# Kernel tuning notes

Hardware: AMD Instinct MI355X
Metric: run time of the kernel (lower is better)

Reference implementation:

```python
import jax, jax.numpy as jnp
import numpy as np

C = 768
H = 12
HD = C // H
SCALE = HD ** -0.5
EPS = 1e-5


def setup_inputs() -> dict:
    key = jax.random.key(0)
    kit = iter(jax.random.split(key, 40))
    r = lambda *s: jax.random.normal(next(kit), s, jnp.float32) * 0.02
    d = dict(
        s_x=jax.random.normal(next(kit), (8, 196, C), jnp.float32),
        t_x=jax.random.normal(next(kit), (8, 1568, C), jnp.float32),
        ln1s_g=jnp.ones(C), ln1s_b=jnp.zeros(C),
        mha_w=r(3 * C, C), mha_b=r(3 * C), mha_ow=r(C, C), mha_ob=r(C),
        ln1t_g=jnp.ones(C), ln1t_b=jnp.zeros(C),
        attn_qkv_w=r(3 * C, C), attn_q_b=r(C), attn_v_b=r(C), attn_pw=r(C, C), attn_pb=r(C),
        lnt2s_g=jnp.ones(C), lnt2s_b=jnp.zeros(C),
        t2s_qw=r(C, C), t2s_qb=r(C), t2s_kvw=r(2 * C, C), t2s_kvb=r(C), t2s_pw=r(C, C), t2s_pb=r(C),
        lns2t_g=jnp.ones(C), lns2t_b=jnp.zeros(C),
        s2t_qw=r(C, C), s2t_qb=r(C), s2t_kvw=r(2 * C, C), s2t_kvb=r(C), s2t_pw=r(C, C), s2t_pb=r(C),
        ln2s_g=jnp.ones(C), ln2s_b=jnp.zeros(C),
        cfc_w=r(4 * C, C), cfc_b=r(4 * C), cproj_w=r(C, 4 * C), cproj_b=r(C),
        ln2t_g=jnp.ones(C), ln2t_b=jnp.zeros(C),
        fc1_w=r(4 * C, C), fc1_b=r(4 * C), fc2_w=r(C, 4 * C), fc2_b=r(C),
    )
    return d


def ln(x, g, b):
    m = x.mean(-1, keepdims=True)
    v = jnp.mean((x - m) ** 2, -1, keepdims=True)
    return (x - m) * jax.lax.rsqrt(v + EPS) * g + b


def heads(x):  # (B, N, C) -> (B, H, N, HD)
    B, N, _ = x.shape
    return x.reshape(B, N, H, HD).transpose(0, 2, 1, 3)


def mhsa(q, k, v):  # (B, H, Nq, HD), (B, H, Nk, HD) -> (B, Nq, C)
    a = jax.nn.softmax(jnp.einsum('bhqd,bhkd->bhqk', q * SCALE, k), axis=-1)
    o = jnp.einsum('bhqk,bhkd->bhqd', a, v)
    B, _, Nq, _ = o.shape
    return o.transpose(0, 2, 1, 3).reshape(B, Nq, C)


def reference(s_x, t_x, ln1s_g, ln1s_b, mha_w, mha_b, mha_ow, mha_ob,
              ln1t_g, ln1t_b, attn_qkv_w, attn_q_b, attn_v_b, attn_pw, attn_pb,
              lnt2s_g, lnt2s_b, t2s_qw, t2s_qb, t2s_kvw, t2s_kvb, t2s_pw, t2s_pb,
              lns2t_g, lns2t_b, s2t_qw, s2t_qb, s2t_kvw, s2t_kvb, s2t_pw, s2t_pb,
              ln2s_g, ln2s_b, cfc_w, cfc_b, cproj_w, cproj_b,
              ln2t_g, ln2t_b, fc1_w, fc1_b, fc2_w, fc2_b):
    # 1) clip self-attention. torch nn.MultiheadAttention (batch_first=False)
    # treats axis 0 of the (B, s_N, C) input as the sequence dim, so we
    # faithfully attend over the batch axis.
    y = ln(s_x, ln1s_g, ln1s_b)
    qkv = y @ mha_w.T + mha_b  # (B, s_N, 3C)
    q, k, v = jnp.split(qkv, 3, axis=-1)
    qt, kt, vt = (a.transpose(1, 0, 2) for a in (q, k, v))  # (s_N, B, C)
    o = mhsa(heads(qt), heads(kt), heads(vt))  # (s_N, B, C)
    o = o @ mha_ow.T + mha_ob
    s_x = s_x + o.transpose(1, 0, 2)

    # 2) video-stream self-attention (qkv_bias=True -> cat(q_b, 0, v_b))
    y = ln(t_x, ln1t_g, ln1t_b)
    qkv_bias = jnp.concatenate([attn_q_b, jnp.zeros_like(attn_v_b), attn_v_b])
    qkv = y @ attn_qkv_w.T + qkv_bias
    q, k, v = jnp.split(qkv, 3, axis=-1)
    o = mhsa(heads(q), heads(k), heads(v))
    t_x = t_x + (o @ attn_pw.T + attn_pb)

    # 3) T2S cross: query from LN(s_x), key/value from (updated, un-normed) t_x
    ys = ln(s_x, lnt2s_g, lnt2s_b)
    q = ys @ t2s_qw.T + t2s_qb
    kv = t_x @ t2s_kvw.T + jnp.concatenate([jnp.zeros_like(t2s_kvb), t2s_kvb])
    k, v = jnp.split(kv, 2, axis=-1)
    o = mhsa(heads(q), heads(k), heads(v))
    s_x = s_x + (o @ t2s_pw.T + t2s_pb)

    # 4) S2T cross: query from LN(t_x), key/value from updated s_x
    yt = ln(t_x, lns2t_g, lns2t_b)
    q = yt @ s2t_qw.T + s2t_qb
    kv = s_x @ s2t_kvw.T + jnp.concatenate([jnp.zeros_like(s2t_kvb), s2t_kvb])
    k, v = jnp.split(kv, 2, axis=-1)
    o = mhsa(heads(q), heads(k), heads(v))
    t_x = t_x + (o @ s2t_pw.T + s2t_pb)

    # 5) clip MLP (QuickGELU)
    y = ln(s_x, ln2s_g, ln2s_b)
    h = y @ cfc_w.T + cfc_b
    h = h * jax.nn.sigmoid(1.702 * h)
    s_x = s_x + (h @ cproj_w.T + cproj_b)

    # 6) video MLP (exact GELU, torch default)
    y = ln(t_x, ln2t_g, ln2t_b)
    h = jax.nn.gelu(y @ fc1_w.T + fc1_b, approximate=False)
    t_x = t_x + (h @ fc2_w.T + fc2_b)
    return (s_x, t_x)
```

## Files before the change

kernel.cpp:

```cpp
#include <hip/hip_runtime.h>
#include <stdint.h>


typedef uint16_t u16;
typedef uint16_t u16x8 __attribute__((ext_vector_type(8)));
typedef uint16_t u16x4 __attribute__((ext_vector_type(4)));
typedef short bf16x8 __attribute__((ext_vector_type(8)));
typedef float f32x4 __attribute__((ext_vector_type(4)));

__device__ __forceinline__ float b2f(u16 u) {
    union { float f; uint32_t i; } x;
    x.i = ((uint32_t)u) << 16;
    return x.f;
}
__device__ __forceinline__ u16 f2b(float f) {
    union { float f; uint32_t i; } x;
    x.f = f;
    uint32_t i = x.i;
    uint32_t r = (i + 0x7FFFu + ((i >> 16) & 1u)) >> 16;
    return (u16)r;
}
__device__ __forceinline__ u16 f2b_trunc(float f) {
    union { float f; uint32_t i; } x;
    x.f = f;
    return (u16)(x.i >> 16);
}

__device__ __forceinline__ void gload16(const u16* g, u16* l) {
    __builtin_amdgcn_global_load_lds(
        (const __attribute__((address_space(1))) uint32_t*)g,
        (__attribute__((address_space(3))) uint32_t*)l, 16, 0, 0);
}

struct CvtAll {
    const float* s[14];
    u16* d[14];
    int cum[15];
};
__global__ __launch_bounds__(256) void cvt_all(CvtAll c) {
    int i = blockIdx.x * 256 + threadIdx.x;
    if (i >= c.cum[14]) return;
    int seg = 0;
    #pragma unroll
    for (int k = 1; k < 14; k++) seg += (i >= c.cum[k]);
    int j = i - c.cum[seg];
    c.d[seg][j] = f2b(c.s[seg][j]);
}

__global__ __launch_bounds__(256) void build_bias_pool(float* __restrict__ dst,
    const float* mha_b, const float* attn_q_b, const float* attn_v_b,
    const float* mha_ob, const float* attn_pb, const float* t2s_kvb,
    const float* t2s_qb, const float* t2s_pb, const float* s2t_qb,
    const float* s2t_kvb, const float* s2t_pb, const float* cfc_b,
    const float* cproj_b, const float* fc1_b, const float* fc2_b) {
    int i = blockIdx.x * 256 + threadIdx.x;
    float v = 0.f;
    if (i < 2304) v = mha_b[i];
    else if (i < 4608) { int j = i - 2304; v = (j < 768) ? attn_q_b[j] : (j < 1536 ? 0.f : attn_v_b[j - 1536]); }
    else if (i < 5376) v = mha_ob[i - 4608];
    else if (i < 6144) v = attn_pb[i - 5376];
    else if (i < 7680) { int j = i - 6144; v = (j < 768) ? 0.f : t2s_kvb[j - 768]; }
    else if (i < 8448) v = t2s_qb[i - 7680];
    else if (i < 9216) v = t2s_pb[i - 8448];
    else if (i < 9984) v = s2t_qb[i - 9216];
    else if (i < 11520) { int j = i - 9984; v = (j < 768) ? 0.f : s2t_kvb[j - 768]; }
    else if (i < 12288) v = s2t_pb[i - 11520];
    else if (i < 15360) v = cfc_b[i - 12288];
    else if (i < 16128) v = cproj_b[i - 15360];
    else if (i < 19200) v = fc1_b[i - 16128];
    else if (i < 19968) v = fc2_b[i - 19200];
    else return;
    dst[i] = v;
}

__device__ __forceinline__ float block_sum(float v, float* red) {
    #pragma unroll
    for (int o = 32; o > 0; o >>= 1) v += __shfl_down(v, o, 64);
    int w = threadIdx.x >> 6, l = threadIdx.x & 63;
    __syncthreads();
    if (l == 0) red[w] = v;
    __syncthreads();
    return red[0] + red[1] + red[2] + red[3];
}

__device__ __forceinline__ void ln_row(const float* xr, const float* g,
                                       const float* bta, u16* yr, float* red) {
    const int t = threadIdx.x;
    float v0 = xr[t], v1 = xr[t + 256], v2 = xr[t + 512];
    float mean = block_sum(v0 + v1 + v2, red) * (1.0f / 768.0f);
    float d0 = v0 - mean, d1 = v1 - mean, d2 = v2 - mean;
    float var = block_sum(d0 * d0 + d1 * d1 + d2 * d2, red) * (1.0f / 768.0f);
    float rs = rsqrtf(var + 1e-5f);
    yr[t]       = f2b(d0 * rs * g[t]       + bta[t]);
    yr[t + 256] = f2b(d1 * rs * g[t + 256] + bta[t + 256]);
    yr[t + 512] = f2b(d2 * rs * g[t + 512] + bta[t + 512]);
}

__global__ __launch_bounds__(256) void ln_dual(
    const float* __restrict__ x, int rows0,
    const float* g0, const float* b0, u16* y0,
    const float* g1, const float* b1, u16* y1) {
    __shared__ float red[4];
    int r = blockIdx.x;
    if (r < rows0) ln_row(x + (size_t)r * 768, g0, b0, y0 + (size_t)r * 768, red);
    else ln_row(x + (size_t)r * 768, g1, b1, y1 + (size_t)(r - rows0) * 768, red);
}

__global__ __launch_bounds__(256) void ln_dual_in(
    const float* __restrict__ xs, const float* __restrict__ xt,
    float* __restrict__ xcopy, int rows0,
    const float* g0, const float* b0, u16* y0,
    const float* g1, const float* b1, u16* y1) {
    __shared__ float red[4];
    int r = blockIdx.x, t = threadIdx.x;
    const float* xr; const float* g; const float* bta; u16* yr;
    if (r < rows0) { xr = xs + (size_t)r * 768; g = g0; bta = b0; yr = y0 + (size_t)r * 768; }
    else { xr = xt + (size_t)(r - rows0) * 768; g = g1; bta = b1; yr = y1 + (size_t)(r - rows0) * 768; }
    float v0 = xr[t], v1 = xr[t + 256], v2 = xr[t + 512];
    float* xc = xcopy + (size_t)r * 768;
    xc[t] = v0; xc[t + 256] = v1; xc[t + 512] = v2;
    float mean = block_sum(v0 + v1 + v2, red) * (1.0f / 768.0f);
    float d0 = v0 - mean, d1 = v1 - mean, d2 = v2 - mean;
    float var = block_sum(d0 * d0 + d1 * d1 + d2 * d2, red) * (1.0f / 768.0f);
    float rs = rsqrtf(var + 1e-5f);
    yr[t]       = f2b(d0 * rs * g[t]       + bta[t]);
    yr[t + 256] = f2b(d1 * rs * g[t + 256] + bta[t + 256]);
    yr[t + 512] = f2b(d2 * rs * g[t + 512] + bta[t + 512]);
}

struct TransP {
    const u16* vp; u16* vt;
    int Nk, Nkp, gx, nb;
    long long vA, vJ;
};
__device__ __forceinline__ void transpose_body(const TransP p, int bid, u16 (*T)[72]) {
    const int x = bid % p.gx, inst = bid / p.gx;
    const int a = inst / 12, h = inst % 12;
    const int t0 = x * 64;
    const int tid = threadIdx.x;
    const int kvl = tid >> 2, dseg = (tid & 3) * 16;
    u16x8 v0 = {}, v1 = {};
    if (t0 + kvl < p.Nk) {
        const u16* src = p.vp + a * p.vA + (long long)(t0 + kvl) * p.vJ + h * 64 + dseg;
        v0 = *(const u16x8*)src;
        v1 = *(const u16x8*)(src + 8);
    }
    *(u16x8*)&T[kvl][dseg]     = v0;
    *(u16x8*)&T[kvl][dseg + 8] = v1;
    __syncthreads();
    const int dl = tid >> 2, kseg = (tid & 3) * 16;
    u16x8 w0, w1;
    #pragma unroll
    for (int j = 0; j < 8; j++) w0[j] = T[kseg + j][dl];
    #pragma unroll
    for (int j = 0; j < 8; j++) w1[j] = T[kseg + 8 + j][dl];
    u16* orow = p.vt + ((size_t)inst * 64 + dl) * p.Nkp + t0 + kseg;
    *(u16x8*)orow = w0;
    *(u16x8*)(orow + 8) = w1;
}
__global__ __launch_bounds__(256) void transpose_pair(TransP p0, TransP p1) {
    __shared__ u16 T[64][72];
    int bid = blockIdx.x;
    if (bid < p0.nb) transpose_body(p0, bid, T);
    else transpose_body(p1, bid - p0.nb, T);
}

struct GemmP {
    const u16* A; const u16* W; const float* bias;
    u16* Cb; float* Cf;
    int M, N, K, gx, nb;
};
template <int MODE, int BM>
__device__ __forceinline__ void gemm_body(const GemmP p, int bid,
                                          u16 (*AsF)[32], u16 (*BsF)[32]) {
    constexpr int MI = BM / 32;
    const int tid = threadIdx.x;
    const int lane = tid & 63;
    const int wid = tid >> 6;
    const int wr = (wid >> 1) * (BM / 2), wc = (wid & 1) * 64;
    const int bx = bid % p.gx, by = bid / p.gx;
    const int m0 = bx * BM, n0 = by * 128;
    const int lr = lane >> 2, lc = (lane & 3) * 8;
    const int fr = lane & 15, fk = (lane >> 4) * 8;
    const int abase = wid * (BM / 4);
    const int bbase = wid * 32;
    f32x4 acc[MI][4] = {};
    for (int k0 = 0; k0 < p.K; k0 += 64) {
        #pragma unroll
        for (int s = 0; s < 2; s++) {
            #pragma unroll
            for (int j = 0; j < BM / 64; j++) {
                int rowa = m0 + abase + j * 16 + lr;
                rowa = rowa < p.M ? rowa : p.M - 1;
                gload16(p.A + (size_t)rowa * p.K + k0 + s * 32 + lc,
                        &AsF[s * 128 + abase + j * 16][0]);
            }
            #pragma unroll
            for (int j = 0; j < 2; j++) {
                gload16(p.W + (size_t)(n0 + bbase + j * 16 + lr) * p.K + k0 + s * 32 + lc,
                        &BsF[s * 128 + bbase + j * 16][0]);
            }
        }
        __syncthreads();
        #pragma unroll
        for (int s = 0; s < 2; s++) {
            bf16x8 a[MI], b[4];
            #pragma unroll
            for (int i = 0; i < MI; i++) a[i] = *(const bf16x8*)&AsF[s * 128 + wr + i * 16 + fr][fk];
            #pragma unroll
            for (int j = 0; j < 4; j++) b[j] = *(const bf16x8*)&BsF[s * 128 + wc + j * 16 + fr][fk];
            #pragma unroll
            for (int i = 0; i < MI; i++)
                #pragma unroll
                for (int j = 0; j < 4; j++)
                    acc[i][j] = __builtin_amdgcn_mfma_f32_16x16x32_bf16(a[i], b[j], acc[i][j], 0, 0, 0);
        }
        __syncthreads();
    }
    const int er = (lane >> 4) * 4;
    #pragma unroll
    for (int i = 0; i < MI; i++) {
        #pragma unroll
        for (int reg = 0; reg < 4; reg++) {
            int r = m0 + wr + i * 16 + er + reg;
            if (r >= p.M) continue;
            #pragma unroll
            for (int j = 0; j < 4; j++) {
                int c = n0 + wc + j * 16 + fr;
                float v = acc[i][j][reg] + p.bias[c];
                size_t idx = (size_t)r * p.N + c;
                if (MODE == 1) {
                    p.Cf[idx] += v;
                } else if (MODE == 4) {
                    float nv = p.Cf[idx] + v;
                    p.Cf[idx] = nv;
                    p.Cb[idx] = f2b(nv);
                } else {
                    if (MODE == 2) v = v / (1.0f + expf(-1.702f * v));
                    if (MODE == 3) v = 0.5f * v * (1.0f + erff(v * 0.70710678118654752f));
                    p.Cb[idx] = f2b(v);
                }
            }
        }
    }
}
template <int M0, int B0, int M1, int B1>
__global__ __launch_bounds__(256) void gemm_pair(GemmP p0, GemmP p1) {
    __shared__ u16 As[2 * 128][32];
    __shared__ u16 Bs[2 * 128][32];
    int bid = blockIdx.x;
    if (bid < p0.nb) gemm_body<M0, B0>(p0, bid, As, Bs);
    else gemm_body<M1, B1>(p1, bid - p0.nb, As, Bs);
}
template <int M0, int B0, int M1, int B1>
__global__ __launch_bounds__(256) void gemm2_trans(GemmP p0, GemmP p1, TransP t0) {
    __shared__ u16 As[2 * 128][32];
    __shared__ u16 Bs[2 * 128][32];
    int bid = blockIdx.x;
    if (bid < p0.nb) gemm_body<M0, B0>(p0, bid, As, Bs);
    else if (bid < p0.nb + p1.nb) gemm_body<M1, B1>(p1, bid - p0.nb, As, Bs);
    else transpose_body(t0, bid - p0.nb - p1.nb, (u16(*)[72])&As[0][0]);
}

template <int MODE>
__global__ __launch_bounds__(512) void gemm256(
    const u16* __restrict__ A, const u16* __restrict__ W,
    const float* __restrict__ bias, u16* __restrict__ Cb,
    float* __restrict__ Cf, int M, int N, int K) {
    __shared__ u16 LA[2][256][64];
    __shared__ u16 LB[2][256][64];
    const int tid = threadIdx.x;
    const int lane = tid & 63, wid = tid >> 6;
    const int wm = wid >> 2, wn = wid & 3;
    int nwg = gridDim.x;
    int q = nwg >> 3, r8 = nwg & 7;
    int xcd = blockIdx.x & 7, orig = blockIdx.x >> 3;
    int bid = (xcd < r8 ? xcd * (q + 1) : r8 * (q + 1) + (xcd - r8) * q) + orig;
    const int gx = M >> 8;
    const int bx = bid % gx, by = bid / gx;
    const int m0 = bx * 256, n0 = by * 256;
    const int srow = tid >> 3;
    const int sgcol = ((tid & 7) * 8) ^ (((tid >> 3) & 7) << 3);
    const u16* Ag = A + (size_t)m0 * K;
    const u16* Bg = W + (size_t)n0 * K;
    const int fr = lane & 15, g = lane >> 4, fk = g * 8;
    const int rsw = (fr & 7) << 3;

    auto stageHalf = [&](u16* half, const u16* gsrc, int rowOff, int kc) {
        #pragma unroll
        for (int c = 0; c < 2; c++) {
            int row = rowOff + c * 64 + srow;
            gload16(gsrc + (size_t)row * K + kc + sgcol,
                    half + c * 4096 + wid * 512);
        }
    };
    auto stage1 = [&](int s, int kc, int which) {
        if (which == 0) stageHalf(&LB[s][0][0],   Bg, 0,   kc);
        else if (which == 1) stageHalf(&LB[s][128][0], Bg, 128, kc);
        else if (which == 2) stageHalf(&LA[s][0][0],   Ag, 0,   kc);
        else stageHalf(&LA[s][128][0], Ag, 128, kc);
    };

    f32x4 acc[8][4] = {};
    const int NT = K >> 6;
    stage1(0, 0, 0); stage1(0, 0, 1); stage1(0, 0, 2); stage1(0, 0, 3);

    for (int kt = 0; kt < NT; kt++) {
        const int cur = kt & 1;
        const int kn = (kt + 1) << 6;
        const bool pf = (kt + 1 < NT);
        asm volatile("s_waitcnt vmcnt(2)" ::: "memory");
        __builtin_amdgcn_s_barrier();
        bf16x8 bfr[4][2];
        #pragma unroll
        for (int fj = 0; fj < 4; fj++)
            #pragma unroll
            for (int ks = 0; ks < 2; ks++)
                bfr[fj][ks] = *(const bf16x8*)&LB[cur][wn * 64 + fj * 16 + fr][(ks * 32 + fk) ^ rsw];
        #pragma unroll
        for (int ph = 0; ph < 2; ph++) {
            bf16x8 afr[2][2];
            #pragma unroll
            for (int i2 = 0; i2 < 2; i2++)
                #pragma unroll
                for (int ks = 0; ks < 2; ks++)
                    afr[i2][ks] = *(const bf16x8*)&LA[cur][(ph * 2 + i2) * 32 + wm * 16 + fr][(ks * 32 + fk) ^ rsw];
            if (pf) stage1(cur ^ 1, kn, ph);
            __builtin_amdgcn_s_setprio(1);
            #pragma unroll
            for (int i2 = 0; i2 < 2; i2++)
                #pragma unroll
                for (int ks = 0; ks < 2; ks++)
                    #pragma unroll
                    for (int fj = 0; fj < 4; fj++)
                        acc[ph * 2 + i2][fj] = __builtin_amdgcn_mfma_f32_16x16x32_bf16(
                            afr[i2][ks], bfr[fj][ks], acc[ph * 2 + i2][fj], 0, 0, 0);
            __builtin_amdgcn_s_setprio(0);
        }
        if (pf) asm volatile("s_waitcnt vmcnt(4)" ::: "memory");
        else    asm volatile("s_waitcnt vmcnt(0)" ::: "memory");
        __builtin_amdgcn_s_barrier();
        #pragma unroll
        for (int ph = 2; ph < 4; ph++) {
            bf16x8 afr[2][2];
            #pragma unroll
            for (int i2 = 0; i2 < 2; i2++)
                #pragma unroll
                for (int ks = 0; ks < 2; ks++)
                    afr[i2][ks] = *(const bf16x8*)&LA[cur][(ph * 2 + i2) * 32 + wm * 16 + fr][(ks * 32 + fk) ^ rsw];
            if (pf) stage1(cur ^ 1, kn, ph);
            __builtin_amdgcn_s_setprio(1);
            #pragma unroll
            for (int i2 = 0; i2 < 2; i2++)
                #pragma unroll
                for (int ks = 0; ks < 2; ks++)
                    #pragma unroll
                    for (int fj = 0; fj < 4; fj++)
                        acc[ph * 2 + i2][fj] = __builtin_amdgcn_mfma_f32_16x16x32_bf16(
                            afr[i2][ks], bfr[fj][ks], acc[ph * 2 + i2][fj], 0, 0, 0);
            __builtin_amdgcn_s_setprio(0);
        }
    }
    const int er = g * 4;
    #pragma unroll
    for (int fi = 0; fi < 8; fi++) {
        #pragma unroll
        for (int reg = 0; reg < 4; reg++) {
            int rr = m0 + fi * 32 + wm * 16 + er + reg;
            #pragma unroll
            for (int fj = 0; fj < 4; fj++) {
                int c = n0 + wn * 64 + fj * 16 + fr;
                float v = acc[fi][fj][reg] + bias[c];
                size_t idx = (size_t)rr * N + c;
                if (MODE == 1) {
                    Cf[idx] += v;
                } else if (MODE == 4) {
                    float nv = Cf[idx] + v;
                    Cf[idx] = nv;
                    Cb[idx] = f2b(nv);
                } else {
                    if (MODE == 2) v = v / (1.0f + expf(-1.702f * v));
                    if (MODE == 3) v = 0.5f * v * (1.0f + erff(v * 0.70710678118654752f));
                    Cb[idx] = f2b(v);
                }
            }
        }
    }
}

struct FlashP {
    const u16* qp; const u16* kp; const u16* vt; u16* op;
    int Nq, Nk, Nkp, gx, nb;
    long long qA, qI, kA, kJ, oA, oI;
};
__device__ __forceinline__ void flash_body(const FlashP p, int bid,
    u16 (*Ks)[64][64], u16 (*Vs)[64][64], u16 (*Ps)[16][64]) {
    const int x = bid % p.gx, inst = bid / p.gx;
    const int a = inst / 12, h = inst % 12;
    const int tid = threadIdx.x, lane = tid & 63, w = tid >> 6;
    const int fr = lane & 15, g = lane >> 4, fk = g * 8;
    const int f3s = (fr & 7) << 3;
    const u16* qb = p.qp + a * p.qA + h * 64;
    const u16* kb = p.kp + a * p.kA + h * 64;
    const u16* vtb = p.vt + (size_t)inst * 64 * p.Nkp;
    const int q0 = x * 64 + w * 16;

    bf16x8 qf[2];
    {
        u16x8 raw0 = {}, raw1 = {};
        int qr = q0 + fr;
        if (qr < p.Nq) {
            const u16* qrp = qb + (long long)qr * p.qI;
            raw0 = *(const u16x8*)(qrp + fk);
            raw1 = *(const u16x8*)(qrp + 32 + fk);
        }
        const float QS = 0.125f * 1.44269504088896340736f;
        u16x8 s0, s1;
        #pragma unroll
        for (int e = 0; e < 8; e++) {
            s0[e] = f2b(b2f(raw0[e]) * QS);
            s1[e] = f2b(b2f(raw1[e]) * QS);
        }
        qf[0] = *(bf16x8*)&s0;
        qf[1] = *(bf16x8*)&s1;
    }
    float mrun = -1e30f, lrun = 0.f;
    f32x4 o[4] = {};

    const int l = lane;
    const int srow = w * 8 + (l >> 3);
    const int sdcol = ((l & 7) * 8) ^ (((l >> 3) & 7) << 3);

    auto STAGE = [&](int s, int t0) {
        #pragma unroll
        for (int c = 0; c < 2; c++) {
            int row = c * 32 + srow;
            int kr = t0 + row; if (kr >= p.Nk) kr = p.Nk - 1;
            gload16(kb + (long long)kr * p.kJ + sdcol, &Ks[s][0][0] + c * 2048 + w * 512);
            gload16(vtb + (size_t)row * p.Nkp + t0 + sdcol, &Vs[s][0][0] + c * 2048 + w * 512);
        }
    };

    const int nt = (p.Nk + 63) >> 6;
    STAGE(0, 0);
    for (int it = 0; it < nt; ++it) {
        const int t0 = it << 6;
        const int cur = it & 1;
        if (it + 1 < nt) {
            STAGE(cur ^ 1, t0 + 64);
            asm volatile("s_waitcnt vmcnt(4)" ::: "memory");
        } else {
            asm volatile("s_waitcnt vmcnt(0)" ::: "memory");
        }
        __builtin_amdgcn_s_barrier();

        f32x4 s[4] = {};
        __builtin_amdgcn_s_setprio(1);
        #pragma unroll
        for (int hh = 0; hh < 4; hh++) {
            bf16x8 k0f = *(const bf16x8*)&Ks[cur][hh * 16 + fr][fk ^ f3s];
            bf16x8 k1f = *(const bf16x8*)&Ks[cur][hh * 16 + fr][(32 + fk) ^ f3s];
            s[hh] = __builtin_amdgcn_mfma_f32_16x16x32_bf16(k0f, qf[0], s[hh], 0, 0, 0);
            s[hh] = __builtin_amdgcn_mfma_f32_16x16x32_bf16(k1f, qf[1], s[hh], 0, 0, 0);
        }
        __builtin_amdgcn_s_setprio(0);

        if (t0 + 64 > p.Nk) {
            #pragma unroll
            for (int hh = 0; hh < 4; hh++)
                #pragma unroll
                for (int r = 0; r < 4; r++)
                    if (t0 + hh * 16 + 4 * g + r >= p.Nk) s[hh][r] = -1e30f;
        }
        float a0 = fmaxf(fmaxf(s[0][0], s[0][1]), s[0][2]);
        float a1 = fmaxf(fmaxf(s[0][3], s[1][0]), s[1][1]);
        float a2 = fmaxf(fmaxf(s[1][2], s[1][3]), s[2][0]);
        float a3 = fmaxf(fmaxf(s[2][1], s[2][2]), s[2][3]);
        float a4 = fmaxf(fmaxf(s[3][0], s[3][1]), s[3][2]);
        float b0 = fmaxf(fmaxf(a0, a1), a2);
        float b1 = fmaxf(fmaxf(a3, a4), s[3][3]);
        float lmax = fmaxf(b0, b1);
        lmax = fmaxf(lmax, __shfl_xor(lmax, 16, 64));
        lmax = fmaxf(lmax, __shfl_xor(lmax, 32, 64));
        if (!__all(lmax <= mrun + 8.0f)) {
            float mn = fmaxf(mrun, lmax);
            float sf = exp2f(mrun - mn);
            mrun = mn;
            lrun *= sf;
            float sfo[4];
            #pragma unroll
            for (int r = 0; r < 4; r++) sfo[r] = __shfl(sf, g * 4 + r, 64);
            #pragma unroll
            for (int dt = 0; dt < 4; dt++)
                #pragma unroll
                for (int r = 0; r < 4; r++) o[dt][r] *= sfo[r];
        }
        float pp[4][4];
        float ps = 0.f;
        #pragma unroll
        for (int hh = 0; hh < 4; hh++)
            #pragma unroll
            for (int r = 0; r < 4; r++) {
                pp[hh][r] = exp2f(s[hh][r] - mrun);
                ps += pp[hh][r];
            }
        ps += __shfl_xor(ps, 16, 64);
        ps += __shfl_xor(ps, 32, 64);
        lrun += ps;
        #pragma unroll
        for (int hh = 0; hh < 4; hh++) {
            u16x4 pk;
            #pragma unroll
            for (int r = 0; r < 4; r++) pk[r] = f2b_trunc(pp[hh][r]);
            *(u16x4*)&Ps[w][fr][(hh * 16 + g * 4) ^ f3s] = pk;
        }
        bf16x8 pa0 = *(const bf16x8*)&Ps[w][fr][fk ^ f3s];
        bf16x8 pa1 = *(const bf16x8*)&Ps[w][fr][(32 + fk) ^ f3s];
        __builtin_amdgcn_s_setprio(1);
        #pragma unroll
        for (int dt = 0; dt < 4; dt++) {
            bf16x8 vf0 = *(const bf16x8*)&Vs[cur][dt * 16 + fr][fk ^ f3s];
            bf16x8 vf1 = *(const bf16x8*)&Vs[cur][dt * 16 + fr][(32 + fk) ^ f3s];
            o[dt] = __builtin_amdgcn_mfma_f32_16x16x32_bf16(pa0, vf0, o[dt], 0, 0, 0);
            o[dt] = __builtin_amdgcn_mfma_f32_16x16x32_bf16(pa1, vf1, o[dt], 0, 0, 0);
        }
        __builtin_amdgcn_s_setprio(0);
        __builtin_amdgcn_s_barrier();
    }
    float rcp = 1.0f / lrun;
    #pragma unroll
    for (int r = 0; r < 4; r++) {
        float rr = __shfl(rcp, g * 4 + r, 64);
        int qq = q0 + g * 4 + r;
        if (qq >= p.Nq) continue;
        u16* orow = p.op + a * p.oA + (long long)qq * p.oI + h * 64;
        #pragma unroll
        for (int dt = 0; dt < 4; dt++)
            orow[dt * 16 + fr] = f2b(o[dt][r] * rr);
    }
}
__global__ __launch_bounds__(256) void flash_pair(FlashP p0, FlashP p1) {
    __shared__ u16 Ks[2][64][64];
    __shared__ u16 Vs[2][64][64];
    __shared__ u16 Ps[4][16][64];
    int bid = blockIdx.x;
    if (bid < p0.nb) flash_body(p0, bid, Ks, Vs, Ps);
    else flash_body(p1, bid - p0.nb, Ks, Vs, Ps);
}

extern "C" void kernel_launch(void* const* d_in, const int* in_sizes, int n_in,
                              void* d_out, int out_size, void* d_ws, size_t ws_size,
                              hipStream_t stream) {
    const int B = 8, sN = 196, tN = 1568;
    const int Ms = B * sN;
    const int Mt = B * tN;
    const int n_sf = Ms * 768;
    const int n_tf = Mt * 768;
    (void)n_in; (void)out_size; (void)ws_size;

    const bool dict_order = (in_sizes[0] == n_sf);
    auto IN = [&](int di, int ai) -> const float* {
        return (const float*)d_in[dict_order ? di : ai];
    };
    const float* in_sx      = IN(0, 35);
    const float* in_tx      = IN(1, 42);
    const float* ln1s_g     = IN(2, 14);
    const float* ln1s_b     = IN(3, 13);
    const float* mha_w      = IN(4, 28);
    const float* mha_b      = IN(5, 25);
    const float* mha_ow     = IN(6, 27);
    const float* mha_ob     = IN(7, 26);
    const float* ln1t_g     = IN(8, 16);
    const float* ln1t_b     = IN(9, 15);
    const float* attn_qkv_w = IN(10, 3);
    const float* attn_q_b   = IN(11, 2);
    const float* attn_v_b   = IN(12, 4);
    const float* attn_pw    = IN(13, 1);
    const float* attn_pb    = IN(14, 0);
    const float* lnt2s_g    = IN(15, 24);
    const float* lnt2s_b    = IN(16, 23);
    const float* t2s_qw     = IN(17, 41);
    const float* t2s_qb     = IN(18, 40);
    const float* t2s_kvw    = IN(19, 37);
    const float* t2s_kvb    = IN(20, 36);
    const float* t2s_pw     = IN(21, 39);
    const float* t2s_pb     = IN(22, 38);
    const float* lns2t_g    = IN(23, 22);
    const float* lns2t_b    = IN(24, 21);
    const float* s2t_qw     = IN(25, 34);
    const float* s2t_qb     = IN(26, 33);
    const float* s2t_kvw    = IN(27, 30);
    const float* s2t_kvb    = IN(28, 29);
    const float* s2t_pw     = IN(29, 32);
    const float* s2t_pb     = IN(30, 31);
    const float* ln2s_g     = IN(31, 18);
    const float* ln2s_b     = IN(32, 17);
    const float* cfc_w      = IN(33, 6);
    const float* cfc_b      = IN(34, 5);
    const float* cproj_w    = IN(35, 8);
    const float* cproj_b    = IN(36, 7);
    const float* ln2t_g     = IN(37, 20);
    const float* ln2t_b     = IN(38, 19);
    const float* fc1_w      = IN(39, 10);
    const float* fc1_b      = IN(40, 9);
    const float* fc2_w      = IN(41, 12);
    const float* fc2_b      = IN(42, 11);

    float* s_f = (float*)d_out;
    float* t_f = (float*)d_out + n_sf;

    char* ws = (char*)d_ws;
    size_t off = 0;
    auto take = [&](size_t bytes) { size_t o = off; off += (bytes + 255) & ~(size_t)255; return o; };
    float* biasP = (float*)(ws + take(19968 * 4));
    u16*   yb    = (u16*)(ws + take((size_t)(Ms + Mt) * 768 * 2));
    u16*   bufA  = (u16*)(ws + take((size_t)Mt * 3072 * 2));
    u16*   bufS  = (u16*)(ws + take((size_t)Mt * 768 * 2));
    u16*   bufB  = (u16*)(ws + take((size_t)Mt * 768 * 2));
    u16*   sxb   = (u16*)(ws + take((size_t)Ms * 768 * 2));
    u16*   vtb_t = (u16*)(ws + take((size_t)96 * 64 * 1600 * 2));
    u16*   yb_s  = yb;
    u16*   yb_t  = yb + (size_t)Ms * 768;
    u16*   vtb_s = yb;
    auto wtake = [&](size_t nelem) { return (u16*)(ws + take(nelem * 2)); };
    u16 *W_mha   = wtake(2304 * 768), *W_mhao  = wtake(768 * 768);
    u16 *W_qkv   = wtake(2304 * 768), *W_attnp = wtake(768 * 768);
    u16 *W_t2sq  = wtake(768 * 768),  *W_t2skv = wtake(1536 * 768), *W_t2sp = wtake(768 * 768);
    u16 *W_s2tq  = wtake(768 * 768),  *W_s2tkv = wtake(1536 * 768), *W_s2tp = wtake(768 * 768);
    u16 *W_cfc   = wtake(3072 * 768), *W_cproj = wtake(768 * 3072);
    u16 *W_fc1   = wtake(3072 * 768), *W_fc2   = wtake(768 * 3072);

    const int B_MHA = 0, B_QKV = 2304, B_MHAO = 4608, B_ATTNP = 5376;
    const int B_T2SKV = 6144, B_T2SQ = 7680, B_T2SP = 8448, B_S2TQ = 9216;
    const int B_S2TKV = 9984, B_S2TP = 11520, B_CFC = 12288, B_CPROJ = 15360;
    const int B_FC1 = 16128, B_FC2 = 19200;

    auto cdiv = [](int a, int b) { return (a + b - 1) / b; };

    {
        CvtAll c;
        const float* ss[14] = { mha_w, mha_ow, attn_qkv_w, attn_pw, t2s_qw, t2s_kvw, t2s_pw,
                                s2t_qw, s2t_kvw, s2t_pw, cfc_w, cproj_w, fc1_w, fc2_w };
        u16* dd[14] = { W_mha, W_mhao, W_qkv, W_attnp, W_t2sq, W_t2skv, W_t2sp,
                        W_s2tq, W_s2tkv, W_s2tp, W_cfc, W_cproj, W_fc1, W_fc2 };
        int nn[14] = { 2304*768, 768*768, 2304*768, 768*768, 768*768, 1536*768, 768*768,
                       768*768, 1536*768, 768*768, 3072*768, 768*3072, 3072*768, 768*3072 };
        int cum = 0;
        for (int k = 0; k < 14; k++) { c.s[k] = ss[k]; c.d[k] = dd[k]; c.cum[k] = cum; cum += nn[k]; }
        c.cum[14] = cum;
        cvt_all<<<cdiv(cum, 256), 256, 0, stream>>>(c);
    }
    build_bias_pool<<<78, 256, 0, stream>>>(biasP,
        mha_b, attn_q_b, attn_v_b, mha_ob, attn_pb, t2s_kvb, t2s_qb, t2s_pb,
        s2t_qb, s2t_kvb, s2t_pb, cfc_b, cproj_b, fc1_b, fc2_b);

    auto GP = [&](const u16* A, const u16* W, const float* bias, u16* Cb, float* Cf,
                  int M, int N, int K, int BM) {
        GemmP p; p.A = A; p.W = W; p.bias = bias; p.Cb = Cb; p.Cf = Cf;
        p.M = M; p.N = N; p.K = K; p.gx = (M + BM - 1) / BM; p.nb = p.gx * (N / 128);
        return p;
    };
    auto FPm = [&](const u16* qp, const u16* kp, const u16* vt, u16* op,
                   int Nq, int Nk, int Nkp, int insts,
                   long long qA, long long qI, long long kA, long long kJ,
                   long long oA, long long oI) {
        FlashP p; p.qp = qp; p.kp = kp; p.vt = vt; p.op = op;
        p.Nq = Nq; p.Nk = Nk; p.Nkp = Nkp; p.gx = (Nq + 63) / 64;
        p.nb = p.gx * insts;
        p.qA = qA; p.qI = qI; p.kA = kA; p.kJ = kJ; p.oA = oA; p.oI = oI;
        return p;
    };
    auto TP = [&](const u16* vp, u16* vt, int Nk, int Nkp, long long vA, long long vJ, int insts) {
        TransP p; p.vp = vp; p.vt = vt; p.Nk = Nk; p.Nkp = Nkp;
        p.gx = (Nk + 63) / 64; p.nb = p.gx * insts; p.vA = vA; p.vJ = vJ;
        return p;
    };

    ln_dual_in<<<Ms + Mt, 256, 0, stream>>>(in_sx, in_tx, (float*)d_out, Ms,
        ln1s_g, ln1s_b, yb_s, ln1t_g, ln1t_b, yb_t);

    gemm256<0><<<49 * (2304 / 256), 512, 0, stream>>>(yb_t, W_qkv, biasP + B_QKV, bufA, (float*)0, Mt, 2304, 768);
    {
        GemmP p0 = GP(yb_s, W_mha, biasP + B_MHA, bufS, 0, Ms, 2304, 768, 64);
        GemmP pz = p0; pz.nb = 0;
        gemm_pair<0, 64, 0, 64><<<p0.nb, 256, 0, stream>>>(p0, pz);
    }
    {
        TransP p0 = TP(bufS + 1536, vtb_s, 8, 64, 2304LL, (long long)sN * 2304, sN * 12);
        TransP p1 = TP(bufA + 1536, vtb_t, tN, 1600, (long long)tN * 2304, 2304LL, B * 12);
        transpose_pair<<<p0.nb + p1.nb, 256, 0, stream>>>(p0, p1);
    }
    {
        FlashP p0 = FPm(bufS, bufS + 768, vtb_s, sxb, 8, 8, 64, sN * 12,
                        2304LL, (long long)sN * 2304, 2304LL, (long long)sN * 2304,
                        768LL, (long long)sN * 768);
        FlashP p1 = FPm(bufA, bufA + 768, vtb_t, bufB, tN, tN, 1600, B * 12,
                        (long long)tN * 2304, 2304LL, (long long)tN * 2304, 2304LL,
                        (long long)tN * 768, 768LL);
        flash_pair<<<p0.nb + p1.nb, 256, 0, stream>>>(p0, p1);
    }
    {
        GemmP p0 = GP(sxb, W_mhao, biasP + B_MHAO, 0, s_f, Ms, 768, 768, 64);
        GemmP p1 = GP(bufB, W_attnp, biasP + B_ATTNP, yb_t, t_f, Mt, 768, 768, 128);
        gemm_pair<1, 64, 4, 128><<<p0.nb + p1.nb, 256, 0, stream>>>(p0, p1);
    }
    ln_dual<<<Ms + Mt, 256, 0, stream>>>((const float*)d_out, Ms,
        lnt2s_g, lnt2s_b, yb_s, lns2t_g, lns2t_b, bufB);
    gemm256<0><<<49 * (1536 / 256), 512, 0, stream>>>(yb_t, W_t2skv, biasP + B_T2SKV, bufA, (float*)0, Mt, 1536, 768);
    {
        GemmP p0 = GP(bufB, W_s2tq, biasP + B_S2TQ, bufS, 0, Mt, 768, 768, 128);
        GemmP p1 = GP(yb_s, W_t2sq, biasP + B_T2SQ, sxb, 0, Ms, 768, 768, 64);
        TransP t0 = TP(bufA + 768, vtb_t, tN, 1600, (long long)tN * 1536, 1536LL, B * 12);
        gemm2_trans<0, 128, 0, 64><<<p0.nb + p1.nb + t0.nb, 256, 0, stream>>>(p0, p1, t0);
    }
    {
        FlashP p0 = FPm(sxb, bufA, vtb_t, yb_s, sN, tN, 1600, B * 12,
                        (long long)sN * 768, 768LL, (long long)tN * 1536, 1536LL,
                        (long long)sN * 768, 768LL);
        FlashP pz = p0; pz.nb = 0;
        flash_pair<<<p0.nb, 256, 0, stream>>>(p0, pz);
    }
    {
        GemmP p0 = GP(yb_s, W_t2sp, biasP + B_T2SP, sxb, s_f, Ms, 768, 768, 64);
        GemmP pz = p0; pz.nb = 0;
        gemm_pair<4, 64, 4, 64><<<p0.nb, 256, 0, stream>>>(p0, pz);
    }
    ln_dual<<<Ms, 256, 0, stream>>>((const float*)d_out, Ms,
        ln2s_g, ln2s_b, yb_s, ln2s_g, ln2s_b, yb_s);
    {
        GemmP p0 = GP(sxb, W_s2tkv, biasP + B_S2TKV, bufB, 0, Ms, 1536, 768, 64);
        GemmP p1 = GP(yb_s, W_cfc, biasP + B_CFC, yb_t, 0, Ms, 3072, 768, 64);
        gemm_pair<0, 64, 2, 64><<<p0.nb + p1.nb, 256, 0, stream>>>(p0, p1);
    }
    {
        GemmP p0 = GP(yb_t, W_cproj, biasP + B_CPROJ, 0, s_f, Ms, 768, 3072, 64);
        GemmP pz = p0; pz.nb = 0;
        TransP t0 = TP(bufB + 768, bufA, sN, 256, (long long)sN * 1536, 1536LL, B * 12);
        gemm2_trans<1, 64, 1, 64><<<p0.nb + t0.nb, 256, 0, stream>>>(p0, pz, t0);
    }
    {
        FlashP p0 = FPm(bufS, bufB, bufA, yb, tN, sN, 256, B * 12,
                        (long long)tN * 768, 768LL, (long long)sN * 1536, 1536LL,
                        (long long)tN * 768, 768LL);
        FlashP pz = p0; pz.nb = 0;
        flash_pair<<<p0.nb, 256, 0, stream>>>(p0, pz);
    }
    {
        GemmP p0 = GP(yb, W_s2tp, biasP + B_S2TP, 0, t_f, Mt, 768, 768, 128);
        GemmP pz = p0; pz.nb = 0;
        gemm_pair<1, 128, 1, 128><<<p0.nb, 256, 0, stream>>>(p0, pz);
    }
    ln_dual<<<Mt, 256, 0, stream>>>(t_f, 0,
        ln2t_g, ln2t_b, yb_t, ln2t_g, ln2t_b, yb_t);
    gemm256<3><<<49 * (3072 / 256), 512, 0, stream>>>(yb_t, W_fc1, biasP + B_FC1, bufA, (float*)0, Mt, 3072, 768);
    {
        GemmP p0 = GP(bufA, W_fc2, biasP + B_FC2, 0, t_f, Mt, 768, 3072, 128);
        GemmP pz = p0; pz.nb = 0;
        gemm_pair<1, 128, 1, 128><<<p0.nb, 256, 0, stream>>>(p0, pz);
    }
}
```

Baseline: 929.6 us.

## Generalize 256x256 GEMM to multi-problem launches with row clamping and use it broadly

Turns the 256x256-tile GEMM into a device body that takes a parameter struct and clamps A rows and masks stores for ragged M. A tri-problem launcher can then batch up to three GEMMs in one grid. Most remaining 128-tile GEMMs (qkv plus mha, the attention projections, t2s kv with the two queries, s2t projection, fc2) move onto it. The V transpose that was fused into a GEMM launch becomes its own launch, and the flash P packing now uses v_cvt_pk_bf16_f32 (round-to-nearest) instead of truncation. Risks include wasted tile work on small M (Ms=1568 rows fits 256 poorly), fewer blocks for N=768 GEMMs, and an extra launch.

```diff
diff --git a/kernel.cpp b/kernel.cpp
--- a/kernel.cpp
+++ b/kernel.cpp
@@ -5,6 +5,7 @@
 typedef uint16_t u16;
 typedef uint16_t u16x8 __attribute__((ext_vector_type(8)));
 typedef uint16_t u16x4 __attribute__((ext_vector_type(4)));
+typedef uint32_t u32x2 __attribute__((ext_vector_type(2)));
 typedef short bf16x8 __attribute__((ext_vector_type(8)));
 typedef float f32x4 __attribute__((ext_vector_type(4)));
 
@@ -19,11 +20,6 @@
     uint32_t i = x.i;
     uint32_t r = (i + 0x7FFFu + ((i >> 16) & 1u)) >> 16;
     return (u16)r;
-}
-__device__ __forceinline__ u16 f2b_trunc(float f) {
-    union { float f; uint32_t i; } x;
-    x.f = f;
-    return (u16)(x.i >> 16);
 }
 
 __device__ __forceinline__ void gload16(const u16* g, u16* l) {
@@ -170,6 +166,7 @@
     u16* Cb; float* Cf;
     int M, N, K, gx, nb;
 };
+
 template <int MODE, int BM>
 __device__ __forceinline__ void gemm_body(const GemmP p, int bid,
                                           u16 (*AsF)[32], u16 (*BsF)[32]) {
@@ -263,42 +260,38 @@
 }
 
 template <int MODE>
-__global__ __launch_bounds__(512) void gemm256(
-    const u16* __restrict__ A, const u16* __restrict__ W,
-    const float* __restrict__ bias, u16* __restrict__ Cb,
-    float* __restrict__ Cf, int M, int N, int K) {
-    __shared__ u16 LA[2][256][64];
-    __shared__ u16 LB[2][256][64];
+__device__ __forceinline__ void g256_body(const GemmP p, int bid, u16* LA, u16* LB) {
     const int tid = threadIdx.x;
     const int lane = tid & 63, wid = tid >> 6;
     const int wm = wid >> 2, wn = wid & 3;
-    int nwg = gridDim.x;
-    int q = nwg >> 3, r8 = nwg & 7;
-    int xcd = blockIdx.x & 7, orig = blockIdx.x >> 3;
-    int bid = (xcd < r8 ? xcd * (q + 1) : r8 * (q + 1) + (xcd - r8) * q) + orig;
-    const int gx = M >> 8;
-    const int bx = bid % gx, by = bid / gx;
+    const int bx = bid % p.gx, by = bid / p.gx;
     const int m0 = bx * 256, n0 = by * 256;
     const int srow = tid >> 3;
     const int sgcol = ((tid & 7) * 8) ^ (((tid >> 3) & 7) << 3);
-    const u16* Ag = A + (size_t)m0 * K;
-    const u16* Bg = W + (size_t)n0 * K;
+    const int K = p.K, M = p.M;
+    const u16* Ag = p.A;
+    const u16* Bg = p.W + (size_t)n0 * K;
     const int fr = lane & 15, g = lane >> 4, fk = g * 8;
     const int rsw = (fr & 7) << 3;
 
-    auto stageHalf = [&](u16* half, const u16* gsrc, int rowOff, int kc) {
-        #pragma unroll
-        for (int c = 0; c < 2; c++) {
-            int row = rowOff + c * 64 + srow;
-            gload16(gsrc + (size_t)row * K + kc + sgcol,
-                    half + c * 4096 + wid * 512);
-        }
-    };
     auto stage1 = [&](int s, int kc, int which) {
-        if (which == 0) stageHalf(&LB[s][0][0],   Bg, 0,   kc);
-        else if (which == 1) stageHalf(&LB[s][128][0], Bg, 128, kc);
-        else if (which == 2) stageHalf(&LA[s][0][0],   Ag, 0,   kc);
-        else stageHalf(&LA[s][128][0], Ag, 128, kc);
+        if (which < 2) {
+            #pragma unroll
+            for (int c = 0; c < 2; c++) {
+                int rl = which * 128 + c * 64 + srow;
+                gload16(Bg + (size_t)rl * K + kc + sgcol,
+                        LB + s * 16384 + which * 8192 + c * 4096 + wid * 512);
+            }
+        } else {
+            int hf = which - 2;
+            #pragma unroll
+            for (int c = 0; c < 2; c++) {
+                int rg = m0 + hf * 128 + c * 64 + srow;
+                rg = rg < M ? rg : M - 1;
+                gload16(Ag + (size_t)rg * K + kc + sgcol,
+                        LA + s * 16384 + hf * 8192 + c * 4096 + wid * 512);
+            }
+        }
     };
 
     f32x4 acc[8][4] = {};
@@ -316,7 +309,7 @@
         for (int fj = 0; fj < 4; fj++)
             #pragma unroll
             for (int ks = 0; ks < 2; ks++)
-                bfr[fj][ks] = *(const bf16x8*)&LB[cur][wn * 64 + fj * 16 + fr][(ks * 32 + fk) ^ rsw];
+                bfr[fj][ks] = *(const bf16x8*)&LB[cur * 16384 + (wn * 64 + fj * 16 + fr) * 64 + ((ks * 32 + fk) ^ rsw)];
         #pragma unroll
         for (int ph = 0; ph < 2; ph++) {
             bf16x8 afr[2][2];
@@ -324,7 +317,7 @@
             for (int i2 = 0; i2 < 2; i2++)
                 #pragma unroll
                 for (int ks = 0; ks < 2; ks++)
-                    afr[i2][ks] = *(const bf16x8*)&LA[cur][(ph * 2 + i2) * 32 + wm * 16 + fr][(ks * 32 + fk) ^ rsw];
+                    afr[i2][ks] = *(const bf16x8*)&LA[cur * 16384 + ((ph * 2 + i2) * 32 + wm * 16 + fr) * 64 + ((ks * 32 + fk) ^ rsw)];
             if (pf) stage1(cur ^ 1, kn, ph);
             __builtin_amdgcn_s_setprio(1);
             #pragma unroll
@@ -347,7 +340,7 @@
             for (int i2 = 0; i2 < 2; i2++)
                 #pragma unroll
                 for (int ks = 0; ks < 2; ks++)
-                    afr[i2][ks] = *(const bf16x8*)&LA[cur][(ph * 2 + i2) * 32 + wm * 16 + fr][(ks * 32 + fk) ^ rsw];
+                    afr[i2][ks] = *(const bf16x8*)&LA[cur * 16384 + ((ph * 2 + i2) * 32 + wm * 16 + fr) * 64 + ((ks * 32 + fk) ^ rsw)];
             if (pf) stage1(cur ^ 1, kn, ph);
             __builtin_amdgcn_s_setprio(1);
             #pragma unroll
@@ -367,25 +360,38 @@
         #pragma unroll
         for (int reg = 0; reg < 4; reg++) {
             int rr = m0 + fi * 32 + wm * 16 + er + reg;
+            if (rr >= M) continue;
             #pragma unroll
             for (int fj = 0; fj < 4; fj++) {
                 int c = n0 + wn * 64 + fj * 16 + fr;
-                float v = acc[fi][fj][reg] + bias[c];
-                size_t idx = (size_t)rr * N + c;
+                float v = acc[fi][fj][reg] + p.bias[c];
+                size_t idx = (size_t)rr * p.N + c;
                 if (MODE == 1) {
-                    Cf[idx] += v;
+                    p.Cf[idx] += v;
                 } else if (MODE == 4) {
-                    float nv = Cf[idx] + v;
-                    Cf[idx] = nv;
-                    Cb[idx] = f2b(nv);
+                    float nv = p.Cf[idx] + v;
+                    p.Cf[idx] = nv;
+                    p.Cb[idx] = f2b(nv);
                 } else {
                     if (MODE == 2) v = v / (1.0f + expf(-1.702f * v));
                     if (MODE == 3) v = 0.5f * v * (1.0f + erff(v * 0.70710678118654752f));
-                    Cb[idx] = f2b(v);
+                    p.Cb[idx] = f2b(v);
                 }
             }
         }
     }
+}
+template <int M0, int M1, int M2>
+__global__ __launch_bounds__(512) void gemm256_tri(GemmP p0, GemmP p1, GemmP p2) {
+    __shared__ u16 LA[2 * 256 * 64];
+    __shared__ u16 LB[2 * 256 * 64];
+    int nwg = gridDim.x;
+    int q = nwg >> 3, r8 = nwg & 7;
+    int xcd = blockIdx.x & 7, orig = blockIdx.x >> 3;
+    int bid = (xcd < r8 ? xcd * (q + 1) : r8 * (q + 1) + (xcd - r8) * q) + orig;
+    if (bid < p0.nb) g256_body<M0>(p0, bid, LA, LB);
+    else if (bid < p0.nb + p1.nb) g256_body<M1>(p1, bid - p0.nb, LA, LB);
+    else g256_body<M2>(p2, bid - p0.nb - p1.nb, LA, LB);
 }
 
 struct FlashP {
@@ -509,10 +515,11 @@
         lrun += ps;
         #pragma unroll
         for (int hh = 0; hh < 4; hh++) {
-            u16x4 pk;
-            #pragma unroll
-            for (int r = 0; r < 4; r++) pk[r] = f2b_trunc(pp[hh][r]);
-            *(u16x4*)&Ps[w][fr][(hh * 16 + g * 4) ^ f3s] = pk;
+            uint32_t plo, phi;
+            asm("v_cvt_pk_bf16_f32 %0, %1, %2" : "=v"(plo) : "v"(pp[hh][0]), "v"(pp[hh][1]));
+            asm("v_cvt_pk_bf16_f32 %0, %1, %2" : "=v"(phi) : "v"(pp[hh][2]), "v"(pp[hh][3]));
+            u32x2 pk; pk[0] = plo; pk[1] = phi;
+            *(u32x2*)&Ps[w][fr][(hh * 16 + g * 4) ^ f3s] = pk;
         }
         bf16x8 pa0 = *(const bf16x8*)&Ps[w][fr][fk ^ f3s];
         bf16x8 pa1 = *(const bf16x8*)&Ps[w][fr][(32 + fk) ^ f3s];
@@ -660,6 +667,13 @@
         p.M = M; p.N = N; p.K = K; p.gx = (M + BM - 1) / BM; p.nb = p.gx * (N / 128);
         return p;
     };
+    auto GP256 = [&](const u16* A, const u16* W, const float* bias, u16* Cb, float* Cf,
+                     int M, int N, int K) {
+        GemmP p; p.A = A; p.W = W; p.bias = bias; p.Cb = Cb; p.Cf = Cf;
+        p.M = M; p.N = N; p.K = K; p.gx = (M + 255) / 256; p.nb = p.gx * (N / 256);
+        return p;
+    };
+    auto ZERO = [&](GemmP p) { GemmP z = p; z.nb = 0; return z; };
     auto FPm = [&](const u16* qp, const u16* kp, const u16* vt, u16* op,
                    int Nq, int Nk, int Nkp, int insts,
                    long long qA, long long qI, long long kA, long long kJ,
@@ -679,11 +693,10 @@
     ln_dual_in<<<Ms + Mt, 256, 0, stream>>>(in_sx, in_tx, (float*)d_out, Ms,
         ln1s_g, ln1s_b, yb_s, ln1t_g, ln1t_b, yb_t);
 
-    gemm256<0><<<49 * (2304 / 256), 512, 0, stream>>>(yb_t, W_qkv, biasP + B_QKV, bufA, (float*)0, Mt, 2304, 768);
-    {
-        GemmP p0 = GP(yb_s, W_mha, biasP + B_MHA, bufS, 0, Ms, 2304, 768, 64);
-        GemmP pz = p0; pz.nb = 0;
-        gemm_pair<0, 64, 0, 64><<<p0.nb, 256, 0, stream>>>(p0, pz);
+    {
+        GemmP p0 = GP256(yb_t, W_qkv, biasP + B_QKV, bufA, 0, Mt, 2304, 768);
+        GemmP p1 = GP256(yb_s, W_mha, biasP + B_MHA, bufS, 0, Ms, 2304, 768);
+        gemm256_tri<0, 0, 0><<<p0.nb + p1.nb, 512, 0, stream>>>(p0, p1, ZERO(p0));
     }
     {
         TransP p0 = TP(bufS + 1536, vtb_s, 8, 64, 2304LL, (long long)sN * 2304, sN * 12);
@@ -700,18 +713,22 @@
         flash_pair<<<p0.nb + p1.nb, 256, 0, stream>>>(p0, p1);
     }
     {
-        GemmP p0 = GP(sxb, W_mhao, biasP + B_MHAO, 0, s_f, Ms, 768, 768, 64);
-        GemmP p1 = GP(bufB, W_attnp, biasP + B_ATTNP, yb_t, t_f, Mt, 768, 768, 128);
-        gemm_pair<1, 64, 4, 128><<<p0.nb + p1.nb, 256, 0, stream>>>(p0, p1);
+        GemmP p0 = GP256(bufB, W_attnp, biasP + B_ATTNP, yb_t, t_f, Mt, 768, 768);
+        GemmP p1 = GP256(sxb, W_mhao, biasP + B_MHAO, 0, s_f, Ms, 768, 768);
+        gemm256_tri<4, 1, 1><<<p0.nb + p1.nb, 512, 0, stream>>>(p0, p1, ZERO(p1));
     }
     ln_dual<<<Ms + Mt, 256, 0, stream>>>((const float*)d_out, Ms,
         lnt2s_g, lnt2s_b, yb_s, lns2t_g, lns2t_b, bufB);
-    gemm256<0><<<49 * (1536 / 256), 512, 0, stream>>>(yb_t, W_t2skv, biasP + B_T2SKV, bufA, (float*)0, Mt, 1536, 768);
-    {
-        GemmP p0 = GP(bufB, W_s2tq, biasP + B_S2TQ, bufS, 0, Mt, 768, 768, 128);
-        GemmP p1 = GP(yb_s, W_t2sq, biasP + B_T2SQ, sxb, 0, Ms, 768, 768, 64);
-        TransP t0 = TP(bufA + 768, vtb_t, tN, 1600, (long long)tN * 1536, 1536LL, B * 12);
-        gemm2_trans<0, 128, 0, 64><<<p0.nb + p1.nb + t0.nb, 256, 0, stream>>>(p0, p1, t0);
+    {
+        GemmP p0 = GP256(yb_t, W_t2skv, biasP + B_T2SKV, bufA, 0, Mt, 1536, 768);
+        GemmP p1 = GP256(bufB, W_s2tq, biasP + B_S2TQ, bufS, 0, Mt, 768, 768);
+        GemmP p2 = GP256(yb_s, W_t2sq, biasP + B_T2SQ, sxb, 0, Ms, 768, 768);
+        gemm256_tri<0, 0, 0><<<p0.nb + p1.nb + p2.nb, 512, 0, stream>>>(p0, p1, p2);
+    }
+    {
+        TransP p0 = TP(bufA + 768, vtb_t, tN, 1600, (long long)tN * 1536, 1536LL, B * 12);
+        TransP pz = p0; pz.nb = 0;
+        transpose_pair<<<p0.nb, 256, 0, stream>>>(p0, pz);
     }
     {
         FlashP p0 = FPm(sxb, bufA, vtb_t, yb_s, sN, tN, 1600, B * 12,
@@ -722,8 +739,7 @@
     }
     {
         GemmP p0 = GP(yb_s, W_t2sp, biasP + B_T2SP, sxb, s_f, Ms, 768, 768, 64);
-        GemmP pz = p0; pz.nb = 0;
-        gemm_pair<4, 64, 4, 64><<<p0.nb, 256, 0, stream>>>(p0, pz);
+        gemm_pair<4, 64, 4, 64><<<p0.nb, 256, 0, stream>>>(p0, ZERO(p0));
     }
     ln_dual<<<Ms, 256, 0, stream>>>((const float*)d_out, Ms,
         ln2s_g, ln2s_b, yb_s, ln2s_g, ln2s_b, yb_s);
@@ -734,9 +750,8 @@
     }
     {
         GemmP p0 = GP(yb_t, W_cproj, biasP + B_CPROJ, 0, s_f, Ms, 768, 3072, 64);
-        GemmP pz = p0; pz.nb = 0;
         TransP t0 = TP(bufB + 768, bufA, sN, 256, (long long)sN * 1536, 1536LL, B * 12);
-        gemm2_trans<1, 64, 1, 64><<<p0.nb + t0.nb, 256, 0, stream>>>(p0, pz, t0);
+        gemm2_trans<1, 64, 1, 64><<<p0.nb + t0.nb, 256, 0, stream>>>(p0, ZERO(p0), t0);
     }
     {
         FlashP p0 = FPm(bufS, bufB, bufA, yb, tN, sN, 256, B * 12,
@@ -746,16 +761,17 @@
         flash_pair<<<p0.nb, 256, 0, stream>>>(p0, pz);
     }
     {
-        GemmP p0 = GP(yb, W_s2tp, biasP + B_S2TP, 0, t_f, Mt, 768, 768, 128);
-        GemmP pz = p0; pz.nb = 0;
-        gemm_pair<1, 128, 1, 128><<<p0.nb, 256, 0, stream>>>(p0, pz);
+        GemmP p0 = GP256(yb, W_s2tp, biasP + B_S2TP, 0, t_f, Mt, 768, 768);
+        gemm256_tri<1, 1, 1><<<p0.nb, 512, 0, stream>>>(p0, ZERO(p0), ZERO(p0));
     }
     ln_dual<<<Mt, 256, 0, stream>>>(t_f, 0,
         ln2t_g, ln2t_b, yb_t, ln2t_g, ln2t_b, yb_t);
-    gemm256<3><<<49 * (3072 / 256), 512, 0, stream>>>(yb_t, W_fc1, biasP + B_FC1, bufA, (float*)0, Mt, 3072, 768);
-    {
-        GemmP p0 = GP(bufA, W_fc2, biasP + B_FC2, 0, t_f, Mt, 768, 3072, 128);
-        GemmP pz = p0; pz.nb = 0;
-        gemm_pair<1, 128, 1, 128><<<p0.nb, 256, 0, stream>>>(p0, pz);
-    }
-}
+    {
+        GemmP p0 = GP256(yb_t, W_fc1, biasP + B_FC1, bufA, 0, Mt, 3072, 768);
+        gemm256_tri<3, 3, 3><<<p0.nb, 512, 0, stream>>>(p0, ZERO(p0), ZERO(p0));
+    }
+    {
+        GemmP p0 = GP256(bufA, W_fc2, biasP + B_FC2, 0, t_f, Mt, 768, 3072);
+        gemm256_tri<1, 1, 1><<<p0.nb, 512, 0, stream>>>(p0, ZERO(p0), ZERO(p0));
+    }
+}
```

After: 966.4 us. +4.0%, slower.
